# Kernel tuning notes

Hardware: AMD Instinct MI355X
Metric: run time of the kernel (lower is better)

## Reference

```python
import jax, jax.numpy as jnp
import numpy as np

B, N, DIM = 8, 4096, 512
H, DH = 8, 64
INNER = H * DH
MIN_FREQ = 1.0 / 64
SCALE = 1.0
ROT_DIM = DH // 2  # 32, per spatial axis
EPS = 1e-5


def setup_inputs() -> dict:
    key = jax.random.key(0)
    ks = jax.random.split(key, 6)
    x = jax.random.normal(ks[0], (B, N, DIM), dtype=jnp.float32)
    pos = jax.random.uniform(ks[1], (B, N, 2), dtype=jnp.float32)
    W_qkv = jax.random.normal(ks[2], (3 * INNER, DIM), dtype=jnp.float32) * (1.0 / DH)
    gamma_k = jnp.ones((DH,), jnp.float32)
    beta_k = jnp.zeros((DH,), jnp.float32)
    gamma_v = jnp.ones((DH,), jnp.float32)
    beta_v = jnp.zeros((DH,), jnp.float32)
    W_out = jax.random.normal(ks[3], (DIM, INNER), dtype=jnp.float32) * (1.0 / np.sqrt(INNER))
    b_out = jnp.zeros((DIM,), jnp.float32)
    return {"x": x, "pos": pos, "W_qkv": W_qkv, "gamma_k": gamma_k, "beta_k": beta_k,
            "gamma_v": gamma_v, "beta_v": beta_v, "W_out": W_out, "b_out": b_out}


def _layernorm(t, gamma, beta):
    mu = jnp.mean(t, axis=-1, keepdims=True)
    var = jnp.var(t, axis=-1, keepdims=True)
    return (t - mu) * jax.lax.rsqrt(var + EPS) * gamma + beta


def _rotate_half(t):
    # '... (j d) -> ... j d' with j=2, then cat(-x2, x1)
    d = t.shape[-1] // 2
    x1, x2 = t[..., :d], t[..., d:]
    return jnp.concatenate((-x2, x1), axis=-1)


def _apply_rot(t, freqs):
    return t * jnp.cos(freqs) + _rotate_half(t) * jnp.sin(freqs)


def _freqs(coord):
    # coord: [b, n]; inv_freq over rotary half-dim
    inv_freq = 1.0 / (10000.0 ** (jnp.arange(0, ROT_DIM, 2, dtype=jnp.float32) / ROT_DIM))
    t = coord * (SCALE / MIN_FREQ)
    f = t[..., None] * inv_freq  # [b, n, ROT_DIM//2]
    return jnp.concatenate((f, f), axis=-1)[:, None, :, :]  # [b, 1, n, ROT_DIM]


def reference(x, pos, W_qkv, gamma_k, beta_k, gamma_v, beta_v, W_out, b_out):
    b, n, _ = x.shape
    qkv = x @ W_qkv.T  # [b, n, 3*INNER]
    q, k, v = jnp.split(qkv, 3, axis=-1)
    split = lambda t: t.reshape(b, n, H, DH).transpose(0, 2, 1, 3)  # b h n d
    q, k, v = split(q), split(k), split(v)

    # Galerkin: LayerNorm on K and V over head dim
    k = _layernorm(k, gamma_k, beta_k)
    v = _layernorm(v, gamma_v, beta_v)

    # 2D rotary on q, k: first half of head dim uses x-coords, second half y-coords
    fx, fy = _freqs(pos[..., 0]), _freqs(pos[..., 1])
    rot2d = lambda t: jnp.concatenate(
        (_apply_rot(t[..., :ROT_DIM], fx), _apply_rot(t[..., ROT_DIM:], fy)), axis=-1)
    q = rot2d(q)
    k = rot2d(k)

    # Associative linear attention: (K^T V) then Q @ (.) / n
    dots = jnp.einsum('bhnd,bhne->bhde', k, v)  # [b, h, d, d]
    out = jnp.einsum('bhnd,bhde->bhne', q, dots) * (1.0 / n)
    out = out.transpose(0, 2, 1, 3).reshape(b, n, INNER)
    return out @ W_out.T + b_out
```

## Files before the change

### kernel.cpp

```cpp
#include <hip/hip_runtime.h>
#include <math.h>

#define NB 8
#define NN 4096
#define NDIM 512
#define NH 8
#define NDH 64
#define QKVC 1536
#define NROWS (NB * NN)
#define EPSF 1e-5f
#define INV_N (1.0f / 4096.0f)
#define L2_10K_16 0.8304820237218406f

typedef __bf16 bf16x8_t __attribute__((ext_vector_type(8)));
typedef float f32x4_t __attribute__((ext_vector_type(4)));
typedef unsigned short u16x8 __attribute__((ext_vector_type(8)));

__device__ inline unsigned short f2bf(float f) {
    unsigned u = __builtin_bit_cast(unsigned, f);
    u += 0x7fff + ((u >> 16) & 1);
    return (unsigned short)(u >> 16);
}
__device__ inline float bf2f(unsigned short u) {
    unsigned v = (unsigned)u << 16;
    return __builtin_bit_cast(float, v);
}

#define GLOAD_LDS16(g, s) __builtin_amdgcn_global_load_lds(                    \
    (const __attribute__((address_space(1))) void*)(g),                        \
    (__attribute__((address_space(3))) void*)(s), 16, 0, 0)

#define VMCNT4 asm volatile("s_waitcnt vmcnt(4)" ::: "memory")
#define VMCNT3 asm volatile("s_waitcnt vmcnt(3)" ::: "memory")
#define VMCNT0 asm volatile("s_waitcnt vmcnt(0)" ::: "memory")
#define BARF   { __builtin_amdgcn_s_barrier(); asm volatile("" ::: "memory"); }

__device__ inline void cvt8v(const float* __restrict__ s,
                             unsigned short* __restrict__ d, int i)
{
    float4 a = *(const float4*)(s + i);
    float4 b = *(const float4*)(s + i + 4);
    ushort4 lo, hi;
    lo.x = f2bf(a.x); lo.y = f2bf(a.y); lo.z = f2bf(a.z); lo.w = f2bf(a.w);
    hi.x = f2bf(b.x); hi.y = f2bf(b.y); hi.z = f2bf(b.z); hi.w = f2bf(b.w);
    *(ushort4*)(d + i)     = lo;
    *(ushort4*)(d + i + 4) = hi;
}

__global__ __launch_bounds__(256)
void cvt_all(const float* __restrict__ x,  const float* __restrict__ wq,
             const float* __restrict__ wo,
             unsigned short* __restrict__ xb, unsigned short* __restrict__ wqb,
             unsigned short* __restrict__ wob, float* __restrict__ dots)
{
    const int bid = blockIdx.x, t = threadIdx.x;
    if (bid < 8192) {
        cvt8v(x, xb, (bid * 256 + t) * 8);
    } else if (bid < 8576) {
        cvt8v(wq, wqb, ((bid - 8192) * 256 + t) * 8);
    } else if (bid < 8704) {
        cvt8v(wo, wob, ((bid - 8576) * 256 + t) * 8);
    } else {
        const float4 z = {0.f, 0.f, 0.f, 0.f};
        float4* dp = (float4*)dots + (size_t)((bid - 8704) * 256 + t) * 4;
        dp[0] = z; dp[1] = z; dp[2] = z; dp[3] = z;
    }
}

#define GEMM_CORE(Asrc_, Bsrc_)                                                \
    f32x4_t acc[4][4] = {};                                                    \
    const int fr = lane & 15;                                                  \
    const int fq = lane >> 4;                                                  \
    const int ch0 = ((fq ^ ((fr >> 1) & 3)) << 3);                             \
    const int rl = tid >> 2;                                                   \
    const int cs = (((tid & 3) ^ ((rl >> 1) & 3)) << 3);                       \
    const unsigned short* Asrc = (Asrc_) + (size_t)rl * NDIM + cs;             \
    const unsigned short* Bsrc = (Bsrc_) + (size_t)rl * NDIM + cs;             \
    const int sdst = wave * 512;                                               \
    STG_A(0, 0); STG_A(0, 1); STG_B(0);                                        \
    STG_A(1, 0); STG_A(1, 1); STG_B(1);                                        \
    _Pragma("unroll")                                                          \
    for (int tt = 0; tt < 16; ++tt) {                                          \
        if (tt == 15) VMCNT0; else VMCNT3;                                     \
        BARF;                                                                  \
        if (tt < 14) { STG_A(tt + 2, 0); STG_A(tt + 2, 1); STG_B(tt + 2); }    \
        bf16x8_t af[4], bfr[4];                                                \
        const int ab = (tt % 3) * 12288;                                       \
        const int bb = ab + 8192;                                              \
        _Pragma("unroll")                                                      \
        for (int mi = 0; mi < 4; ++mi)                                         \
            af[mi] = *(const bf16x8_t*)&lds[ab + (warp_m * 64 + mi * 16 + fr) * 32 + ch0]; \
        _Pragma("unroll")                                                      \
        for (int nj = 0; nj < 4; ++nj)                                         \
            bfr[nj] = *(const bf16x8_t*)&lds[bb + (warp_n * 64 + nj * 16 + fr) * 32 + ch0]; \
        __builtin_amdgcn_s_setprio(1);                                         \
        _Pragma("unroll")                                                      \
        for (int mi = 0; mi < 4; ++mi)                                         \
            _Pragma("unroll")                                                  \
            for (int nj = 0; nj < 4; ++nj)                                     \
                acc[mi][nj] = __builtin_amdgcn_mfma_f32_16x16x32_bf16(         \
                    af[mi], bfr[nj], acc[mi][nj], 0, 0, 0);                    \
        __builtin_amdgcn_s_setprio(0);                                         \
    }

#define STG_A(tt, c) GLOAD_LDS16(Asrc + (size_t)((c) * 128) * NDIM + (tt) * 32, \
        &lds[((tt) % 3) * 12288 + ((c) * 4096) + sdst])
#define STG_B(tt)    GLOAD_LDS16(Bsrc + (tt) * 32, \
        &lds[((tt) % 3) * 12288 + 8192 + sdst])

__global__ __launch_bounds__(512, 4)
void gemm_kv_fused(const unsigned short* __restrict__ A,
                   const unsigned short* __restrict__ Bm,
                   const float* __restrict__ pos,
                   const float* __restrict__ gk, const float* __restrict__ bk,
                   const float* __restrict__ gv, const float* __restrict__ bvv,
                   unsigned short* __restrict__ kT,
                   unsigned short* __restrict__ vT)
{
    __shared__ __align__(16) unsigned short lds[36864];

    const int tid  = threadIdx.x;
    const int wave = tid >> 6;
    const int lane = tid & 63;

    int flat = blockIdx.y * 8 + blockIdx.x;
    flat = (flat & 7) * 128 + (flat >> 3);
    const int bx = flat & 7;
    const int by = flat >> 3;
    const int m0 = by * 256;
    const int n0 = bx * 128;

    const int warp_m = wave >> 1;
    const int warp_n = wave & 1;

    GEMM_CORE(A + (size_t)m0 * NDIM, Bm + (size_t)n0 * NDIM)

    const int nc = n0 + warp_n * 64;
    const int isK = (nc < 512);
    const int c  = lane & 15;
    const int g4 = (lane >> 4) * 4;
    const int mrow0 = m0 + warp_m * 64;
    const int h = (nc >> 6) & 7;

    {
        const float* gamma = isK ? gk : gv;
        const float* beta  = isK ? bk : bvv;
        float gm[4], bt[4];
        #pragma unroll
        for (int j = 0; j < 4; ++j) { gm[j] = gamma[j * 16 + c]; bt[j] = beta[j * 16 + c]; }
        #pragma unroll
        for (int i = 0; i < 4; ++i)
            #pragma unroll
            for (int r = 0; r < 4; ++r) {
                float t0 = acc[i][0][r], t1 = acc[i][1][r];
                float t2 = acc[i][2][r], t3 = acc[i][3][r];
                float s  = t0 + t1 + t2 + t3;
                float ss = t0*t0 + t1*t1 + t2*t2 + t3*t3;
                #pragma unroll
                for (int msk = 1; msk < 16; msk <<= 1) {
                    s  += __shfl_xor(s,  msk, 64);
                    ss += __shfl_xor(ss, msk, 64);
                }
                const float mu = s * (1.0f / 64.0f);
                const float rs = rsqrtf(ss * (1.0f / 64.0f) - mu * mu + EPSF);
                acc[i][0][r] = (t0 - mu) * rs * gm[0] + bt[0];
                acc[i][1][r] = (t1 - mu) * rs * gm[1] + bt[1];
                acc[i][2][r] = (t2 - mu) * rs * gm[2] + bt[2];
                acc[i][3][r] = (t3 - mu) * rs * gm[3] + bt[3];
            }
    }
    if (isK) {
        const float Kc = 64.0f * exp2f(-(float)c * L2_10K_16);
        #pragma unroll
        for (int i = 0; i < 4; ++i)
            #pragma unroll
            for (int r = 0; r < 4; ++r) {
                const int row = mrow0 + i * 16 + g4 + r;
                const float2 p = ((const float2*)pos)[row];
                float sx, cx, sy, cy;
                __sincosf(p.x * Kc, &sx, &cx);
                __sincosf(p.y * Kc, &sy, &cy);
                const float t0 = acc[i][0][r], t1 = acc[i][1][r];
                const float t2 = acc[i][2][r], t3 = acc[i][3][r];
                acc[i][0][r] = t0 * cx - t1 * sx;
                acc[i][1][r] = t1 * cx + t0 * sx;
                acc[i][2][r] = t2 * cy - t3 * sy;
                acc[i][3][r] = t3 * cy + t2 * sy;
            }
    }
    unsigned short* T = isK ? kT : vT;
    #pragma unroll
    for (int i = 0; i < 4; ++i) {
        const int row = mrow0 + i * 16 + g4;
        const int bb2 = row >> 12;
        const int nl = row & 4095;
        #pragma unroll
        for (int j = 0; j < 4; ++j) {
            ushort4 o;
            o.x = f2bf(acc[i][j][0]); o.y = f2bf(acc[i][j][1]);
            o.z = f2bf(acc[i][j][2]); o.w = f2bf(acc[i][j][3]);
            *(ushort4*)(T + ((size_t)((bb2 * NH + h) * 64 + j * 16 + c)) * NN + nl) = o;
        }
    }
}

__global__ __launch_bounds__(512, 4)
void gemm_q_fused(const unsigned short* __restrict__ A,
                  const unsigned short* __restrict__ Bm,
                  const float* __restrict__ pos,
                  unsigned short* __restrict__ qb)
{
    __shared__ __align__(16) unsigned short lds[36864];

    const int tid  = threadIdx.x;
    const int wave = tid >> 6;
    const int lane = tid & 63;

    int flat = blockIdx.y * 4 + blockIdx.x;
    flat = (flat & 7) * 64 + (flat >> 3);
    const int bx = flat & 3;
    const int by = flat >> 2;
    const int m0 = by * 256;
    const int n0 = bx * 128;

    const int warp_m = wave >> 1;
    const int warp_n = wave & 1;

    GEMM_CORE(A + (size_t)m0 * NDIM, Bm + (size_t)n0 * NDIM)

    const int nc = n0 + warp_n * 64;
    const int c  = lane & 15;
    const int g4 = (lane >> 4) * 4;
    const int mrow0 = m0 + warp_m * 64;

    {
        const float Kc = 64.0f * exp2f(-(float)c * L2_10K_16);
        #pragma unroll
        for (int i = 0; i < 4; ++i)
            #pragma unroll
            for (int r = 0; r < 4; ++r) {
                const int row = mrow0 + i * 16 + g4 + r;
                const float2 p = ((const float2*)pos)[row];
                float sx, cx, sy, cy;
                __sincosf(p.x * Kc, &sx, &cx);
                __sincosf(p.y * Kc, &sy, &cy);
                const float t0 = acc[i][0][r], t1 = acc[i][1][r];
                const float t2 = acc[i][2][r], t3 = acc[i][3][r];
                acc[i][0][r] = t0 * cx - t1 * sx;
                acc[i][1][r] = t1 * cx + t0 * sx;
                acc[i][2][r] = t2 * cy - t3 * sy;
                acc[i][3][r] = t3 * cy + t2 * sy;
            }
    }
    #pragma unroll
    for (int i = 0; i < 4; ++i)
        #pragma unroll
        for (int j = 0; j < 4; ++j) {
            unsigned short* qp = qb + (size_t)(mrow0 + i * 16 + g4) * NDIM
                               + nc + j * 16 + c;
            #pragma unroll
            for (int r = 0; r < 4; ++r)
                qp[(size_t)r * NDIM] = f2bf(acc[i][j][r]);
        }
}

__global__ __launch_bounds__(512, 4)
void gemm_out_mfma(const unsigned short* __restrict__ qb,
                   const unsigned short* __restrict__ M2b,
                   const float* __restrict__ bias, float* __restrict__ C)
{
    __shared__ __align__(16) unsigned short lds[36864];

    const int tid  = threadIdx.x;
    const int wave = tid >> 6;
    const int lane = tid & 63;

    int flat = blockIdx.y * 4 + blockIdx.x;
    flat = (flat & 7) * 64 + (flat >> 3);
    const int bx = flat & 3;
    const int by = flat >> 2;
    const int m0 = by * 256;
    const int n0 = bx * 128;
    const int b  = m0 >> 12;

    const int warp_m = wave >> 1;
    const int warp_n = wave & 1;

    GEMM_CORE(qb + (size_t)m0 * NDIM,
              M2b + (size_t)b * NDIM * NDIM + (size_t)n0 * NDIM)

    const int c  = lane & 15;
    const int g4 = (lane >> 4) * 4;
    const int mrow0 = m0 + warp_m * 64;
    const int ncol = n0 + warp_n * 64;

    #pragma unroll
    for (int j = 0; j < 4; ++j) {
        const int col = ncol + j * 16 + c;
        const float bb2 = bias[col];
        #pragma unroll
        for (int i = 0; i < 4; ++i) {
            float* cp = C + (size_t)(mrow0 + i * 16 + g4) * NDIM + col;
            #pragma unroll
            for (int r = 0; r < 4; ++r)
                cp[(size_t)r * NDIM] = acc[i][j][r] + bb2;
        }
    }
}

__global__ __launch_bounds__(256)
void dots_mfma(const unsigned short* __restrict__ kT,
               const unsigned short* __restrict__ vT,
               float* __restrict__ dots)
{
    __shared__ __align__(16) unsigned short sk[3][64 * 64];
    __shared__ __align__(16) unsigned short sv[3][64 * 64];
    const int t = threadIdx.x;
    const int w = t >> 6, l = t & 63;
    const int bh = blockIdx.z * NH + blockIdx.y;
    const int n0 = blockIdx.x * 512;

    const int r8 = l >> 3;
    const int cs = ((l & 7) ^ r8) * 8;
    const unsigned short* ksrc = kT + (size_t)(bh * 64 + w * 16 + r8) * NN + n0 + cs;
    const unsigned short* vsrc = vT + (size_t)(bh * 64 + w * 16 + r8) * NN + n0 + cs;

#define STGK(ss, q) GLOAD_LDS16(ksrc + (size_t)(q) * 8 * NN + (ss) * 64, \
        &sk[(ss) % 3][w * 1024 + (q) * 512])
#define STGV(ss, q) GLOAD_LDS16(vsrc + (size_t)(q) * 8 * NN + (ss) * 64, \
        &sv[(ss) % 3][w * 1024 + (q) * 512])

    const int fr = l & 15, fq = l >> 4;
    const int doff = (w >> 1) * 32, eoff = (w & 1) * 32;

    f32x4_t acc[2][2] = {};

    STGK(0, 0); STGK(0, 1); STGV(0, 0); STGV(0, 1);
    STGK(1, 0); STGK(1, 1); STGV(1, 0); STGV(1, 1);

    #pragma unroll
    for (int s = 0; s < 8; ++s) {
        if (s == 7) VMCNT0; else VMCNT4;
        __builtin_amdgcn_s_barrier();
        asm volatile("" ::: "memory");
        if (s < 6) { STGK(s + 2, 0); STGK(s + 2, 1); STGV(s + 2, 0); STGV(s + 2, 1); }
        const int buf = s % 3;
        bf16x8_t ak[2][2], bv[2][2];
        #pragma unroll
        for (int di = 0; di < 2; ++di)
            #pragma unroll
            for (int ks = 0; ks < 2; ++ks)
                ak[di][ks] = *(const bf16x8_t*)
                    &sk[buf][(doff + di * 16 + fr) * 64 + (((ks * 4 + fq) ^ (fr & 7)) * 8)];
        #pragma unroll
        for (int ej = 0; ej < 2; ++ej)
            #pragma unroll
            for (int ks = 0; ks < 2; ++ks)
                bv[ej][ks] = *(const bf16x8_t*)
                    &sv[buf][(eoff + ej * 16 + fr) * 64 + (((ks * 4 + fq) ^ (fr & 7)) * 8)];
        __builtin_amdgcn_s_setprio(1);
        #pragma unroll
        for (int ks = 0; ks < 2; ++ks)
            #pragma unroll
            for (int di = 0; di < 2; ++di)
                #pragma unroll
                for (int ej = 0; ej < 2; ++ej)
                    acc[di][ej] = __builtin_amdgcn_mfma_f32_16x16x32_bf16(
                        ak[di][ks], bv[ej][ks], acc[di][ej], 0, 0, 0);
        __builtin_amdgcn_s_setprio(0);
    }
#undef STGK
#undef STGV

    float* dp = dots + (size_t)bh * 64 * 64;
    const int cc = l & 15;
    const int rr = (l >> 4) * 4;
    #pragma unroll
    for (int di = 0; di < 2; ++di)
        #pragma unroll
        for (int ej = 0; ej < 2; ++ej)
            #pragma unroll
            for (int r = 0; r < 4; ++r)
                atomicAdd(dp + (doff + di * 16 + rr + r) * 64 + eoff + ej * 16 + cc,
                          acc[di][ej][r]);
}

__global__ __launch_bounds__(256)
void dotsw_mfma(const unsigned short* __restrict__ Woutb,
                const float* __restrict__ dots,
                unsigned short* __restrict__ M2b)
{
    __shared__ unsigned short As[128 * 64];
    __shared__ unsigned short Bs[64 * 64];
    const int t = threadIdx.x;
    const int wave = t >> 6;
    const int lane = t & 63;
    const int dp0 = blockIdx.x * 128;
    const int h = blockIdx.y, b = blockIdx.z;

    const int srow = lane >> 3;
    const int scol = (lane & 7) * 8;
    const unsigned short* Ag = Woutb + (size_t)(dp0 + wave * 32 + srow) * NDIM
                             + h * NDH + scol;
    #pragma unroll
    for (int i = 0; i < 4; ++i)
        GLOAD_LDS16(Ag + (size_t)i * 8 * NDIM, As + wave * 2048 + i * 512);

    {
        const float* Dg = dots + (size_t)(b * NH + h) * 4096;
        const int dr = t >> 2;
        const int dc = (t & 3) * 16;
        const float* dgp = Dg + dr * 64 + dc;
        float4 f0 = *(const float4*)(dgp);
        float4 f1 = *(const float4*)(dgp + 4);
        float4 f2 = *(const float4*)(dgp + 8);
        float4 f3 = *(const float4*)(dgp + 12);
        ushort4 o0, o1, o2, o3;
        o0.x = f2bf(f0.x * INV_N); o0.y = f2bf(f0.y * INV_N);
        o0.z = f2bf(f0.z * INV_N); o0.w = f2bf(f0.w * INV_N);
        o1.x = f2bf(f1.x * INV_N); o1.y = f2bf(f1.y * INV_N);
        o1.z = f2bf(f1.z * INV_N); o1.w = f2bf(f1.w * INV_N);
        o2.x = f2bf(f2.x * INV_N); o2.y = f2bf(f2.y * INV_N);
        o2.z = f2bf(f2.z * INV_N); o2.w = f2bf(f2.w * INV_N);
        o3.x = f2bf(f3.x * INV_N); o3.y = f2bf(f3.y * INV_N);
        o3.z = f2bf(f3.z * INV_N); o3.w = f2bf(f3.w * INV_N);
        *(ushort4*)&Bs[dr * 64 + dc]      = o0;
        *(ushort4*)&Bs[dr * 64 + dc + 4]  = o1;
        *(ushort4*)&Bs[dr * 64 + dc + 8]  = o2;
        *(ushort4*)&Bs[dr * 64 + dc + 12] = o3;
    }
    __syncthreads();

    const int wm = (wave >> 1) * 64;
    const int wn = (wave & 1) * 32;
    const int fr = lane & 15;
    const int fq = (lane >> 4) * 8;

    f32x4_t acc[4][2] = {};
    #pragma unroll
    for (int kk = 0; kk < 2; ++kk) {
        bf16x8_t af[4], bf[2];
        #pragma unroll
        for (int i = 0; i < 4; ++i)
            af[i] = *(const bf16x8_t*)&As[(wm + i * 16 + fr) * 64 + kk * 32 + fq];
        #pragma unroll
        for (int j = 0; j < 2; ++j)
            bf[j] = *(const bf16x8_t*)&Bs[(wn + j * 16 + fr) * 64 + kk * 32 + fq];
        #pragma unroll
        for (int i = 0; i < 4; ++i)
            #pragma unroll
            for (int j = 0; j < 2; ++j)
                acc[i][j] = __builtin_amdgcn_mfma_f32_16x16x32_bf16(
                    af[i], bf[j], acc[i][j], 0, 0, 0);
    }

    const int c  = lane & 15;
    const int g4 = (lane >> 4) * 4;
    #pragma unroll
    for (int i = 0; i < 4; ++i)
        #pragma unroll
        for (int j = 0; j < 2; ++j) {
            unsigned short* mp = M2b + ((size_t)(b * NDIM) + dp0 + wm + i * 16 + g4) * NDIM
                               + h * NDH + wn + j * 16 + c;
            #pragma unroll
            for (int r = 0; r < 4; ++r)
                mp[(size_t)r * NDIM] = f2bf(acc[i][j][r]);
        }
}

extern "C" void kernel_launch(void* const* d_in, const int* in_sizes, int n_in,
                              void* d_out, int out_size, void* d_ws, size_t ws_size,
                              hipStream_t stream)
{
    const float* x    = (const float*)d_in[0];
    const float* pos  = (const float*)d_in[1];
    const float* Wqkv = (const float*)d_in[2];
    const float* gk   = (const float*)d_in[3];
    const float* bk   = (const float*)d_in[4];
    const float* gv   = (const float*)d_in[5];
    const float* bv   = (const float*)d_in[6];
    const float* Wout = (const float*)d_in[7];
    const float* bout = (const float*)d_in[8];
    float* out = (float*)d_out;

    float* dots = (float*)d_ws;
    unsigned short* M2b     = (unsigned short*)(dots + (size_t)NB * NH * 64 * 64);
    unsigned short* qb      = M2b + (size_t)NB * NDIM * NDIM;
    unsigned short* kT      = qb + (size_t)NROWS * NDIM;
    unsigned short* vT      = kT + (size_t)NB * NH * NDH * NN;
    unsigned short* xb      = vT + (size_t)NB * NH * NDH * NN;
    unsigned short* Wqkvb   = xb + (size_t)NROWS * NDIM;
    unsigned short* Woutb   = Wqkvb + (size_t)QKVC * NDIM;

    cvt_all<<<dim3(8768), dim3(256), 0, stream>>>(x, Wqkv, Wout, xb, Wqkvb, Woutb, dots);
    gemm_kv_fused<<<dim3(8, NROWS / 256), dim3(512), 0, stream>>>(
        xb, Wqkvb + (size_t)512 * NDIM, pos, gk, bk, gv, bv, kT, vT);
    gemm_q_fused<<<dim3(4, NROWS / 256), dim3(512), 0, stream>>>(
        xb, Wqkvb, pos, qb);
    dots_mfma<<<dim3(NN / 512, NH, NB), dim3(256), 0, stream>>>(kT, vT, dots);
    dotsw_mfma<<<dim3(NDIM / 128, NH, NB), dim3(256), 0, stream>>>(Woutb, dots, M2b);
    gemm_out_mfma<<<dim3(NDIM / 128, NROWS / 256), dim3(512), 0, stream>>>(
        qb, M2b, bout, out);
}
```

Measured before the change: 271.3 us.

## Widen GEMM K-tile to 64 with split-phase prefetch, double-buffer dots kernel

The shared GEMM core now stages 64-wide K tiles instead of 32, so it runs 8 iterations instead of 16. Each tile is split into two half-steps, and the next tile's global-to-LDS loads are issued between fragment reads and MFMAs, with barriers around each half. LDS per block roughly doubles, so launch bounds drop from 4 to 2 blocks per CU, trading occupancy for fewer synchronisations and deeper per-iteration work. The dots kernel moves from a triple-buffered, unrolled pipeline to a rolled double buffer with a full vmcnt(0) wait each step and no priority hints, which exposes more load latency.

```diff
diff --git a/kernel.cpp b/kernel.cpp
--- a/kernel.cpp
+++ b/kernel.cpp
@@ -29,11 +29,6 @@
 #define GLOAD_LDS16(g, s) __builtin_amdgcn_global_load_lds(                    \
     (const __attribute__((address_space(1))) void*)(g),                        \
     (__attribute__((address_space(3))) void*)(s), 16, 0, 0)
-
-#define VMCNT4 asm volatile("s_waitcnt vmcnt(4)" ::: "memory")
-#define VMCNT3 asm volatile("s_waitcnt vmcnt(3)" ::: "memory")
-#define VMCNT0 asm volatile("s_waitcnt vmcnt(0)" ::: "memory")
-#define BARF   { __builtin_amdgcn_s_barrier(); asm volatile("" ::: "memory"); }
 
 __device__ inline void cvt8v(const float* __restrict__ s,
                              unsigned short* __restrict__ d, int i)
@@ -67,48 +62,64 @@
     }
 }
 
-#define GEMM_CORE(Asrc_, Bsrc_)                                                \
+#define STG_A(tt, a) GLOAD_LDS16(Asrc + (size_t)(a) * 64 * NDIM + (tt) * 64,   \
+        &lds[((tt) % 3) * 24576 + (a) * 4096 + wave * 512])
+#define STG_B(tt, bb) GLOAD_LDS16(Bsrc + (size_t)(bb) * 64 * NDIM + (tt) * 64, \
+        &lds[((tt) % 3) * 24576 + 16384 + (bb) * 4096 + wave * 512])
+
+#define GEMM_CORE64(Abase_, Bbase_)                                            \
     f32x4_t acc[4][4] = {};                                                    \
     const int fr = lane & 15;                                                  \
     const int fq = lane >> 4;                                                  \
-    const int ch0 = ((fq ^ ((fr >> 1) & 3)) << 3);                             \
-    const int rl = tid >> 2;                                                   \
-    const int cs = (((tid & 3) ^ ((rl >> 1) & 3)) << 3);                       \
-    const unsigned short* Asrc = (Asrc_) + (size_t)rl * NDIM + cs;             \
-    const unsigned short* Bsrc = (Bsrc_) + (size_t)rl * NDIM + cs;             \
-    const int sdst = wave * 512;                                               \
-    STG_A(0, 0); STG_A(0, 1); STG_B(0);                                        \
-    STG_A(1, 0); STG_A(1, 1); STG_B(1);                                        \
+    const int rc = fr & 7;                                                     \
+    const int wm = warp_m * 64;                                                \
+    const int wn = warp_n * 64;                                                \
+    const int row8 = lane >> 3;                                                \
+    const int csrc = ((lane & 7) ^ row8) * 8;                                  \
+    const unsigned short* Asrc = (Abase_) + (size_t)(wave * 8 + row8) * NDIM + csrc; \
+    const unsigned short* Bsrc = (Bbase_) + (size_t)(wave * 8 + row8) * NDIM + csrc; \
+    STG_A(0, 0); STG_A(0, 1); STG_A(0, 2); STG_A(0, 3);                        \
+    STG_B(0, 0); STG_B(0, 1);                                                  \
+    STG_A(1, 0); STG_A(1, 1); STG_A(1, 2); STG_A(1, 3);                        \
+    STG_B(1, 0); STG_B(1, 1);                                                  \
+    asm volatile("s_waitcnt vmcnt(6)" ::: "memory");                           \
+    __builtin_amdgcn_s_barrier();                                              \
     _Pragma("unroll")                                                          \
-    for (int tt = 0; tt < 16; ++tt) {                                          \
-        if (tt == 15) VMCNT0; else VMCNT3;                                     \
-        BARF;                                                                  \
-        if (tt < 14) { STG_A(tt + 2, 0); STG_A(tt + 2, 1); STG_B(tt + 2); }    \
-        bf16x8_t af[4], bfr[4];                                                \
-        const int ab = (tt % 3) * 12288;                                       \
-        const int bb = ab + 8192;                                              \
+    for (int tt = 0; tt < 8; ++tt) {                                           \
+        const unsigned short* Ab = &lds[(tt % 3) * 24576];                     \
+        const unsigned short* Bb = Ab + 16384;                                 \
         _Pragma("unroll")                                                      \
-        for (int mi = 0; mi < 4; ++mi)                                         \
-            af[mi] = *(const bf16x8_t*)&lds[ab + (warp_m * 64 + mi * 16 + fr) * 32 + ch0]; \
-        _Pragma("unroll")                                                      \
-        for (int nj = 0; nj < 4; ++nj)                                         \
-            bfr[nj] = *(const bf16x8_t*)&lds[bb + (warp_n * 64 + nj * 16 + fr) * 32 + ch0]; \
-        __builtin_amdgcn_s_setprio(1);                                         \
-        _Pragma("unroll")                                                      \
-        for (int mi = 0; mi < 4; ++mi)                                         \
+        for (int kh = 0; kh < 2; ++kh) {                                       \
+            const int ch = (((kh << 2) | fq) ^ rc) * 8;                        \
+            bf16x8_t af[4], bfrag[4];                                          \
+            _Pragma("unroll")                                                  \
+            for (int mi = 0; mi < 4; ++mi)                                     \
+                af[mi] = *(const bf16x8_t*)&Ab[(wm + mi * 16 + fr) * 64 + ch]; \
             _Pragma("unroll")                                                  \
             for (int nj = 0; nj < 4; ++nj)                                     \
-                acc[mi][nj] = __builtin_amdgcn_mfma_f32_16x16x32_bf16(         \
-                    af[mi], bfr[nj], acc[mi][nj], 0, 0, 0);                    \
-        __builtin_amdgcn_s_setprio(0);                                         \
-    }
-
-#define STG_A(tt, c) GLOAD_LDS16(Asrc + (size_t)((c) * 128) * NDIM + (tt) * 32, \
-        &lds[((tt) % 3) * 12288 + ((c) * 4096) + sdst])
-#define STG_B(tt)    GLOAD_LDS16(Bsrc + (tt) * 32, \
-        &lds[((tt) % 3) * 12288 + 8192 + sdst])
-
-__global__ __launch_bounds__(512, 4)
+                bfrag[nj] = *(const bf16x8_t*)&Bb[(wn + nj * 16 + fr) * 64 + ch]; \
+            if (tt < 6) {                                                      \
+                if (kh == 0) { STG_A(tt + 2, 0); STG_A(tt + 2, 1); STG_A(tt + 2, 2); } \
+                else         { STG_A(tt + 2, 3); STG_B(tt + 2, 0); STG_B(tt + 2, 1); } \
+            }                                                                  \
+            __builtin_amdgcn_s_barrier();                                      \
+            __builtin_amdgcn_s_setprio(1);                                     \
+            _Pragma("unroll")                                                  \
+            for (int mi = 0; mi < 4; ++mi)                                     \
+                _Pragma("unroll")                                              \
+                for (int nj = 0; nj < 4; ++nj)                                 \
+                    acc[mi][nj] = __builtin_amdgcn_mfma_f32_16x16x32_bf16(     \
+                        af[mi], bfrag[nj], acc[mi][nj], 0, 0, 0);              \
+            __builtin_amdgcn_s_setprio(0);                                     \
+            if (kh == 1) {                                                     \
+                if (tt < 6)       asm volatile("s_waitcnt vmcnt(6)" ::: "memory"); \
+                else if (tt == 6) asm volatile("s_waitcnt vmcnt(0)" ::: "memory"); \
+            }                                                                  \
+            __builtin_amdgcn_s_barrier();                                      \
+        }                                                                      \
+    }
+
+__global__ __launch_bounds__(512, 2)
 void gemm_kv_fused(const unsigned short* __restrict__ A,
                    const unsigned short* __restrict__ Bm,
                    const float* __restrict__ pos,
@@ -117,11 +128,11 @@
                    unsigned short* __restrict__ kT,
                    unsigned short* __restrict__ vT)
 {
-    __shared__ __align__(16) unsigned short lds[36864];
-
-    const int tid  = threadIdx.x;
-    const int wave = tid >> 6;
-    const int lane = tid & 63;
+    __shared__ __align__(16) unsigned short lds[3 * 24576];
+
+    const int tid  = threadIdx.x; (void)tid;
+    const int wave = threadIdx.x >> 6;
+    const int lane = threadIdx.x & 63;
 
     int flat = blockIdx.y * 8 + blockIdx.x;
     flat = (flat & 7) * 128 + (flat >> 3);
@@ -133,7 +144,7 @@
     const int warp_m = wave >> 1;
     const int warp_n = wave & 1;
 
-    GEMM_CORE(A + (size_t)m0 * NDIM, Bm + (size_t)n0 * NDIM)
+    GEMM_CORE64(A + (size_t)m0 * NDIM, Bm + (size_t)n0 * NDIM)
 
     const int nc = n0 + warp_n * 64;
     const int isK = (nc < 512);
@@ -204,17 +215,17 @@
     }
 }
 
-__global__ __launch_bounds__(512, 4)
+__global__ __launch_bounds__(512, 2)
 void gemm_q_fused(const unsigned short* __restrict__ A,
                   const unsigned short* __restrict__ Bm,
                   const float* __restrict__ pos,
                   unsigned short* __restrict__ qb)
 {
-    __shared__ __align__(16) unsigned short lds[36864];
-
-    const int tid  = threadIdx.x;
-    const int wave = tid >> 6;
-    const int lane = tid & 63;
+    __shared__ __align__(16) unsigned short lds[3 * 24576];
+
+    const int tid  = threadIdx.x; (void)tid;
+    const int wave = threadIdx.x >> 6;
+    const int lane = threadIdx.x & 63;
 
     int flat = blockIdx.y * 4 + blockIdx.x;
     flat = (flat & 7) * 64 + (flat >> 3);
@@ -226,7 +237,7 @@
     const int warp_m = wave >> 1;
     const int warp_n = wave & 1;
 
-    GEMM_CORE(A + (size_t)m0 * NDIM, Bm + (size_t)n0 * NDIM)
+    GEMM_CORE64(A + (size_t)m0 * NDIM, Bm + (size_t)n0 * NDIM)
 
     const int nc = n0 + warp_n * 64;
     const int c  = lane & 15;
@@ -264,16 +275,16 @@
         }
 }
 
-__global__ __launch_bounds__(512, 4)
+__global__ __launch_bounds__(512, 2)
 void gemm_out_mfma(const unsigned short* __restrict__ qb,
                    const unsigned short* __restrict__ M2b,
                    const float* __restrict__ bias, float* __restrict__ C)
 {
-    __shared__ __align__(16) unsigned short lds[36864];
-
-    const int tid  = threadIdx.x;
-    const int wave = tid >> 6;
-    const int lane = tid & 63;
+    __shared__ __align__(16) unsigned short lds[3 * 24576];
+
+    const int tid  = threadIdx.x; (void)tid;
+    const int wave = threadIdx.x >> 6;
+    const int lane = threadIdx.x & 63;
 
     int flat = blockIdx.y * 4 + blockIdx.x;
     flat = (flat & 7) * 64 + (flat >> 3);
@@ -286,8 +297,8 @@
     const int warp_m = wave >> 1;
     const int warp_n = wave & 1;
 
-    GEMM_CORE(qb + (size_t)m0 * NDIM,
-              M2b + (size_t)b * NDIM * NDIM + (size_t)n0 * NDIM)
+    GEMM_CORE64(qb + (size_t)m0 * NDIM,
+                M2b + (size_t)b * NDIM * NDIM + (size_t)n0 * NDIM)
 
     const int c  = lane & 15;
     const int g4 = (lane >> 4) * 4;
@@ -313,8 +324,8 @@
                const unsigned short* __restrict__ vT,
                float* __restrict__ dots)
 {
-    __shared__ __align__(16) unsigned short sk[3][64 * 64];
-    __shared__ __align__(16) unsigned short sv[3][64 * 64];
+    __shared__ __align__(16) unsigned short sk[2][64 * 64];
+    __shared__ __align__(16) unsigned short sv[2][64 * 64];
     const int t = threadIdx.x;
     const int w = t >> 6, l = t & 63;
     const int bh = blockIdx.z * NH + blockIdx.y;
@@ -325,26 +336,22 @@
     const unsigned short* ksrc = kT + (size_t)(bh * 64 + w * 16 + r8) * NN + n0 + cs;
     const unsigned short* vsrc = vT + (size_t)(bh * 64 + w * 16 + r8) * NN + n0 + cs;
 
-#define STGK(ss, q) GLOAD_LDS16(ksrc + (size_t)(q) * 8 * NN + (ss) * 64, \
-        &sk[(ss) % 3][w * 1024 + (q) * 512])
-#define STGV(ss, q) GLOAD_LDS16(vsrc + (size_t)(q) * 8 * NN + (ss) * 64, \
-        &sv[(ss) % 3][w * 1024 + (q) * 512])
+#define STGK(buf, kt, q) GLOAD_LDS16(ksrc + (size_t)(q) * 8 * NN + (kt), \
+        &sk[buf][w * 1024 + (q) * 512])
+#define STGV(buf, kt, q) GLOAD_LDS16(vsrc + (size_t)(q) * 8 * NN + (kt), \
+        &sv[buf][w * 1024 + (q) * 512])
 
     const int fr = l & 15, fq = l >> 4;
     const int doff = (w >> 1) * 32, eoff = (w & 1) * 32;
 
     f32x4_t acc[2][2] = {};
 
-    STGK(0, 0); STGK(0, 1); STGV(0, 0); STGV(0, 1);
-    STGK(1, 0); STGK(1, 1); STGV(1, 0); STGV(1, 1);
-
-    #pragma unroll
+    STGK(0, 0, 0); STGK(0, 0, 1); STGV(0, 0, 0); STGV(0, 0, 1);
+
     for (int s = 0; s < 8; ++s) {
-        if (s == 7) VMCNT0; else VMCNT4;
+        const int buf = s & 1;
+        asm volatile("s_waitcnt vmcnt(0)" ::: "memory");
         __builtin_amdgcn_s_barrier();
-        asm volatile("" ::: "memory");
-        if (s < 6) { STGK(s + 2, 0); STGK(s + 2, 1); STGV(s + 2, 0); STGV(s + 2, 1); }
-        const int buf = s % 3;
         bf16x8_t ak[2][2], bv[2][2];
         #pragma unroll
         for (int di = 0; di < 2; ++di)
@@ -358,7 +365,10 @@
             for (int ks = 0; ks < 2; ++ks)
                 bv[ej][ks] = *(const bf16x8_t*)
                     &sv[buf][(eoff + ej * 16 + fr) * 64 + (((ks * 4 + fq) ^ (fr & 7)) * 8)];
-        __builtin_amdgcn_s_setprio(1);
+        if (s + 1 < 8) {
+            const int nb = buf ^ 1, kt = (s + 1) * 64;
+            STGK(nb, kt, 0); STGK(nb, kt, 1); STGV(nb, kt, 0); STGV(nb, kt, 1);
+        }
         #pragma unroll
         for (int ks = 0; ks < 2; ++ks)
             #pragma unroll
@@ -367,7 +377,6 @@
                 for (int ej = 0; ej < 2; ++ej)
                     acc[di][ej] = __builtin_amdgcn_mfma_f32_16x16x32_bf16(
                         ak[di][ks], bv[ej][ks], acc[di][ej], 0, 0, 0);
-        __builtin_amdgcn_s_setprio(0);
     }
 #undef STGK
 #undef STGV
```

New measurement: 268.0 us. About the same (-1.2%).
